# Performance work log

Hardware: AMD Instinct MI355X
Metric: run time of the kernel (lower is better)

## Reference

```python
import jax, jax.numpy as jnp
import numpy as np

EPS = 1e-5
G, N, H, P, K = 8, 128, 64, 64, 4  # n_groups, d_state, n_heads, head_dim, conv kernel
R = H // G  # heads per group


def _rmsnorm(x, w, eps=EPS):
    return x * jax.lax.rsqrt(jnp.mean(x * x, axis=-1, keepdims=True) + eps) * w


def setup_inputs() -> dict:
    key = jax.random.key(0)
    ks = jax.random.split(key, 8)
    B, L, Dm = 2, 1024, 2048
    d_inner = 2 * Dm                      # 4096
    conv_dim = d_inner + 2 * G * N        # 6144
    proj_dim = 2 * d_inner + 2 * G * N + H  # 10304
    return {
        "hidden_states": jax.random.normal(ks[0], (B, L, Dm), jnp.float32),
        "residual": jax.random.normal(ks[1], (B, L, Dm), jnp.float32),
        "norm_w": jnp.ones((Dm,), jnp.float32),
        "in_proj_w": jax.random.normal(ks[2], (proj_dim, Dm), jnp.float32) * 0.02,
        "conv_w": jax.random.normal(ks[3], (conv_dim, K), jnp.float32) * 0.1,
        "conv_b": jnp.zeros((conv_dim,), jnp.float32),
        "A_log": jnp.log(jnp.arange(1, H + 1, dtype=jnp.float32)),
        "D_param": jnp.ones((H,), jnp.float32),
        "dt_bias": jax.random.uniform(ks[4], (H,), jnp.float32, -4.0, -1.0),
        "gate_norm_w": jnp.ones((d_inner,), jnp.float32),
        "out_proj_w": jax.random.normal(ks[5], (Dm, d_inner), jnp.float32) * 0.02,
    }


def reference(hidden_states, residual, norm_w, in_proj_w, conv_w, conv_b,
              A_log, D_param, dt_bias, gate_norm_w, out_proj_w):
    B, L, Dm = hidden_states.shape
    d_inner = 2 * Dm
    conv_dim = d_inner + 2 * G * N

    # fused residual-add RMSNorm (residual is not None branch)
    h = hidden_states + residual
    new_residual = h
    x = _rmsnorm(h, norm_w)

    # in_proj -> [z | xBC | dt]
    proj = jnp.einsum('bld,ed->ble', x, in_proj_w)
    z = proj[..., :d_inner]
    xBC = proj[..., d_inner:d_inner + conv_dim]
    dt = proj[..., d_inner + conv_dim:]            # [B, L, H]

    # causal depthwise conv1d over xBC, then SiLU
    lhs = jnp.transpose(xBC, (0, 2, 1))            # [B, C, L]
    rhs = conv_w[:, None, :]                       # [C, 1, K]
    conv = jax.lax.conv_general_dilated(
        lhs, rhs, window_strides=(1,), padding=[(K - 1, 0)],
        feature_group_count=conv_dim)
    xBC = jax.nn.silu(jnp.transpose(conv, (0, 2, 1)) + conv_b)

    xs = xBC[..., :d_inner].reshape(B, L, G, R, P)   # per-head inputs
    Bm = xBC[..., d_inner:d_inner + G * N].reshape(B, L, G, N)
    Cm = xBC[..., d_inner + G * N:].reshape(B, L, G, N)

    dt = jax.nn.softplus(dt + dt_bias)               # [B, L, H]
    A = -jnp.exp(A_log)                              # [H]
    dA = jnp.exp(dt * A).reshape(B, L, G, R)
    dtg = dt.reshape(B, L, G, R)

    # time-major for scan
    def step(hst, inp):
        dA_t, dt_t, x_t, B_t, C_t = inp            # [B,G,R], [B,G,R], [B,G,R,P], [B,G,N], [B,G,N]
        dBx = jnp.einsum('bgr,bgn,bgrp->bgrpn', dt_t, B_t, x_t)
        hst = hst * dA_t[..., None, None] + dBx    # [B,G,R,P,N]
        y_t = jnp.einsum('bgrpn,bgn->bgrp', hst, C_t)
        return hst, y_t

    tm = lambda a: jnp.moveaxis(a, 1, 0)
    h0 = jnp.zeros((B, G, R, P, N), hidden_states.dtype)
    _, ys = jax.lax.scan(step, h0, (tm(dA), tm(dtg), tm(xs), tm(Bm), tm(Cm)))
    y = jnp.moveaxis(ys, 0, 1)                     # [B, L, G, R, P]
    y = y + D_param.reshape(G, R)[None, None, :, :, None] * xs
    y = y.reshape(B, L, d_inner)

    # gated RMSNorm then out_proj
    y = _rmsnorm(y * jax.nn.silu(z), gate_norm_w)
    out = jnp.einsum('ble,de->bld', y, out_proj_w)
    return out, new_residual
```

## Files before the change

kernel.cpp:

```cpp
#include <hip/hip_runtime.h>

#define TOK 2048
#define DM 2048
#define DI 4096
#define NG 8
#define NN 128
#define PROJ_D 10304
#define PROJ_P 10496
#define CONV_D 6144
#define LSEQ 1024
#define CHUNK 64
#define NCHUNK 16

typedef unsigned short u16;
typedef __attribute__((ext_vector_type(4))) float f32x4;
typedef __attribute__((ext_vector_type(8))) short s16x8;
typedef __attribute__((ext_vector_type(4))) unsigned short u16x4;

__device__ __forceinline__ u16 f2bf(float f) {
  union { float f; unsigned u; } x; x.f = f;
  unsigned r = (x.u + 0x7FFFu + ((x.u >> 16) & 1u)) >> 16;
  return (u16)r;
}
__device__ __forceinline__ float bf2f(u16 u) {
  union { unsigned u; float f; } x; x.u = ((unsigned)u) << 16; return x.f;
}

__device__ __forceinline__ float blockReduceSum256(float s) {
  __shared__ float red[4];
  #pragma unroll
  for (int o = 32; o > 0; o >>= 1) s += __shfl_down(s, o, 64);
  int lane = threadIdx.x & 63, wid = threadIdx.x >> 6;
  if (lane == 0) red[wid] = s;
  __syncthreads();
  return red[0] + red[1] + red[2] + red[3];
}

__global__ __launch_bounds__(256) void cvt_bf16_pad(const float* __restrict__ src, u16* __restrict__ dst,
                                                    long n_src, long n_dst) {
  long i = ((long)blockIdx.x * 256 + threadIdx.x) * 4;
  if (i >= n_dst) return;
  u16x4 o;
  if (i < n_src) {
    f32x4 v = *(const f32x4*)&src[i];
    o.x = f2bf(v.x); o.y = f2bf(v.y); o.z = f2bf(v.z); o.w = f2bf(v.w);
  } else {
    o.x = 0; o.y = 0; o.z = 0; o.w = 0;
  }
  *(u16x4*)&dst[i] = o;
}

__global__ __launch_bounds__(256) void addnorm_kernel(const float* __restrict__ hs, const float* __restrict__ res,
        const float* __restrict__ w, float* __restrict__ nres, u16* __restrict__ xbf) {
  int row = blockIdx.x;
  size_t base = (size_t)row * DM;
  int tid = threadIdx.x;
  f32x4 h[2];
  float s = 0.f;
  #pragma unroll
  for (int i = 0; i < 2; i++) {
    int off = i * 1024 + tid * 4;
    f32x4 a = *(const f32x4*)&hs[base + off];
    f32x4 b = *(const f32x4*)&res[base + off];
    f32x4 v = a + b;
    h[i] = v;
    *(f32x4*)&nres[base + off] = v;
    s += v.x * v.x + v.y * v.y + v.z * v.z + v.w * v.w;
  }
  s = blockReduceSum256(s);
  float rs = rsqrtf(s * (1.f / DM) + 1e-5f);
  #pragma unroll
  for (int i = 0; i < 2; i++) {
    int off = i * 1024 + tid * 4;
    f32x4 wv = *(const f32x4*)&w[off];
    f32x4 v = h[i];
    u16x4 o;
    o.x = f2bf(v.x * rs * wv.x);
    o.y = f2bf(v.y * rs * wv.y);
    o.z = f2bf(v.z * rs * wv.z);
    o.w = f2bf(v.w * rs * wv.w);
    *(u16x4*)&xbf[base + off] = o;
  }
}

__device__ __forceinline__ void gld_lds16(const void* g, void* l) {
  __builtin_amdgcn_global_load_lds((const __attribute__((address_space(1))) void*)g,
                                   (__attribute__((address_space(3))) void*)l, 16, 0, 0);
}

template <bool BF16OUT>
__global__ __launch_bounds__(512, 4) void gemm32(const u16* __restrict__ A, const u16* __restrict__ Bw,
                                                 void* __restrict__ Cv, int K, int Cstride, int nbx) {
  __shared__ u16 As[3][128][32];
  __shared__ u16 Bs[3][256][32];
  int tid = threadIdx.x;
  int lane = tid & 63, w = tid >> 6;
  int wr = w >> 2, wc = w & 3;
  int cpx = gridDim.x >> 3;
  int bid = blockIdx.x;
  int lb = (bid & 7) * cpx + (bid >> 3);
  int by = lb / nbx, bx = lb - by * nbx;
  size_t m0 = (size_t)by * 128, n0 = (size_t)bx * 256;
  const u16* Ab = A + m0 * K;
  const u16* Bb = Bw + n0 * K;

  f32x4 acc[4][4];
  #pragma unroll
  for (int i = 0; i < 4; ++i)
    #pragma unroll
    for (int j = 0; j < 4; ++j) acc[i][j] = (f32x4){0.f, 0.f, 0.f, 0.f};

  int fr = lane & 15, fq = lane >> 4;
  int lrow = lane >> 2, lg = lane & 3;

  auto S = [&](int kt) {
    int bu = kt % 3;
    {
      int row = w * 16 + lrow;
      int cs = (lg ^ ((row >> 1) & 3)) * 8;
      gld_lds16(Ab + (size_t)row * K + kt * 32 + cs, &As[bu][w * 16][0]);
    }
    #pragma unroll
    for (int j = 0; j < 2; ++j) {
      int row = j * 128 + w * 16 + lrow;
      int cs = (lg ^ ((row >> 1) & 3)) * 8;
      gld_lds16(Bb + (size_t)row * K + kt * 32 + cs, &Bs[bu][j * 128 + w * 16][0]);
    }
  };

  int nkt = K >> 5;
  S(0); S(1);
  asm volatile("s_waitcnt vmcnt(3)" ::: "memory");
  __builtin_amdgcn_s_barrier();

  for (int kt = 0; kt < nkt; ++kt) {
    int bu = kt % 3;
    s16x8 a[4], b[4];
    #pragma unroll
    for (int mi = 0; mi < 4; ++mi) {
      int row = wr * 64 + mi * 16 + fr;
      a[mi] = *(const s16x8*)&As[bu][row][(fq ^ ((row >> 1) & 3)) * 8];
    }
    #pragma unroll
    for (int ni = 0; ni < 4; ++ni) {
      int row = wc * 64 + ni * 16 + fr;
      b[ni] = *(const s16x8*)&Bs[bu][row][(fq ^ ((row >> 1) & 3)) * 8];
    }
    if (kt + 2 < nkt) {
      S(kt + 2);
      asm volatile("s_waitcnt vmcnt(3)" ::: "memory");
    } else {
      asm volatile("s_waitcnt vmcnt(0)" ::: "memory");
    }
    __builtin_amdgcn_s_barrier();
    __builtin_amdgcn_s_setprio(1);
    #pragma unroll
    for (int mi = 0; mi < 4; ++mi)
      #pragma unroll
      for (int ni = 0; ni < 4; ++ni)
        acc[mi][ni] = __builtin_amdgcn_mfma_f32_16x16x32_bf16(a[mi], b[ni], acc[mi][ni], 0, 0, 0);
    __builtin_amdgcn_s_setprio(0);
    __builtin_amdgcn_s_barrier();
  }
  size_t crow0 = m0 + wr * 64 + fq * 4;
  size_t ccol0 = n0 + wc * 64 + fr;
  if constexpr (BF16OUT) {
    u16* C = (u16*)Cv;
    #pragma unroll
    for (int mi = 0; mi < 4; ++mi)
      #pragma unroll
      for (int ni = 0; ni < 4; ++ni)
        #pragma unroll
        for (int j = 0; j < 4; ++j)
          C[(crow0 + mi * 16 + j) * Cstride + ccol0 + ni * 16] = f2bf(acc[mi][ni][j]);
  } else {
    float* C = (float*)Cv;
    #pragma unroll
    for (int mi = 0; mi < 4; ++mi)
      #pragma unroll
      for (int ni = 0; ni < 4; ++ni)
        #pragma unroll
        for (int j = 0; j < 4; ++j)
          C[(crow0 + mi * 16 + j) * Cstride + ccol0 + ni * 16] = acc[mi][ni][j];
  }
}

template <bool BF16OUT>
__global__ __launch_bounds__(512, 2) void gemm8p(const u16* __restrict__ A, const u16* __restrict__ Bw,
                                                 void* __restrict__ Cv, int K, int Cstride, int nbx,
                                                 int nks, size_t part_stride) {
  __shared__ u16 As[2][256][64];
  __shared__ u16 Bs[2][256][64];
  int tid = threadIdx.x;
  int lane = tid & 63, w = tid >> 6;
  int wr = w >> 2, wc = w & 3;
  int cpx = gridDim.x >> 3;
  int bid = blockIdx.x;
  int lb = (bid & 7) * cpx + (bid >> 3);
  int ks = lb % nks;
  int tile = lb / nks;
  int by = tile / nbx, bx = tile - by * nbx;
  int Ks = K / nks;
  int k0 = ks * Ks;
  size_t m0 = (size_t)by * 256, n0 = (size_t)bx * 256;
  const u16* Ab = A + m0 * K;
  const u16* Bb = Bw + n0 * K;

  f32x4 acc[8][4];
  #pragma unroll
  for (int i = 0; i < 8; ++i)
    #pragma unroll
    for (int j = 0; j < 4; ++j) acc[i][j] = (f32x4){0.f, 0.f, 0.f, 0.f};

  int l3 = lane >> 3;
  int colsw = ((lane & 7) ^ l3) << 3;
  int fr = lane & 15, fq = lane >> 4;
  int pc0 = (fq * 8) ^ ((fr & 7) << 3);
  int pc1 = pc0 ^ 32;

  auto S = [&](int kt, int mat, int half) {
    int d = kt & 1;
    const u16* src = mat ? Bb : Ab;
    u16* dstbase = mat ? &Bs[d][0][0] : &As[d][0][0];
    #pragma unroll
    for (int j = 0; j < 2; ++j) {
      int rb = half * 128 + (w * 2 + j) * 8;
      gld_lds16(src + (size_t)(rb + l3) * K + k0 + kt * 64 + colsw, dstbase + rb * 64);
    }
  };

  int nkt = Ks >> 6;
  S(0, 1, 0); S(0, 1, 1); S(0, 0, 0); S(0, 0, 1);
  S(1, 1, 0); S(1, 1, 1);
  asm volatile("s_waitcnt vmcnt(4)" ::: "memory");
  __builtin_amdgcn_s_barrier();

  for (int kt = 0; kt < nkt; ++kt) {
    int d = kt & 1;
    s16x8 b[4][2];
    #pragma unroll
    for (int q = 0; q < 4; ++q) {
      if (q == 0) {
        #pragma unroll
        for (int ni = 0; ni < 4; ++ni) {
          b[ni][0] = *(const s16x8*)&Bs[d][wc * 64 + ni * 16 + fr][pc0];
          b[ni][1] = *(const s16x8*)&Bs[d][wc * 64 + ni * 16 + fr][pc1];
        }
      }
      s16x8 a[2][2];
      #pragma unroll
      for (int mi = 0; mi < 2; ++mi) {
        a[mi][0] = *(const s16x8*)&As[d][wr * 128 + q * 32 + mi * 16 + fr][pc0];
        a[mi][1] = *(const s16x8*)&As[d][wr * 128 + q * 32 + mi * 16 + fr][pc1];
      }
      if (q == 0)      { if (kt + 1 < nkt) S(kt + 1, 0, 0); }
      else if (q == 1) { if (kt + 1 < nkt) S(kt + 1, 0, 1); }
      else if (q == 2) { if (kt + 2 < nkt) S(kt + 2, 1, 0); }
      else {
        if (kt + 2 < nkt) { S(kt + 2, 1, 1); asm volatile("s_waitcnt vmcnt(4)" ::: "memory"); }
        else              { asm volatile("s_waitcnt vmcnt(0)" ::: "memory"); }
      }
      __builtin_amdgcn_s_barrier();
      __builtin_amdgcn_s_setprio(1);
      #pragma unroll
      for (int mi = 0; mi < 2; ++mi)
        #pragma unroll
        for (int ni = 0; ni < 4; ++ni) {
          acc[q * 2 + mi][ni] = __builtin_amdgcn_mfma_f32_16x16x32_bf16(a[mi][0], b[ni][0], acc[q * 2 + mi][ni], 0, 0, 0);
          acc[q * 2 + mi][ni] = __builtin_amdgcn_mfma_f32_16x16x32_bf16(a[mi][1], b[ni][1], acc[q * 2 + mi][ni], 0, 0, 0);
        }
      __builtin_amdgcn_s_setprio(0);
      __builtin_amdgcn_s_barrier();
    }
  }
  size_t crow0 = m0 + wr * 128 + fq * 4;
  size_t ccol0 = n0 + wc * 64 + fr;
  if constexpr (BF16OUT) {
    u16* C = (u16*)Cv;
    #pragma unroll
    for (int mf = 0; mf < 8; ++mf)
      #pragma unroll
      for (int ni = 0; ni < 4; ++ni)
        #pragma unroll
        for (int j = 0; j < 4; ++j)
          C[(crow0 + mf * 16 + j) * Cstride + ccol0 + ni * 16] = f2bf(acc[mf][ni][j]);
  } else {
    float* C = (float*)Cv + (size_t)ks * part_stride;
    #pragma unroll
    for (int mf = 0; mf < 8; ++mf)
      #pragma unroll
      for (int ni = 0; ni < 4; ++ni)
        #pragma unroll
        for (int j = 0; j < 4; ++j)
          C[(crow0 + mf * 16 + j) * Cstride + ccol0 + ni * 16] = acc[mf][ni][j];
  }
}

__global__ __launch_bounds__(256) void reduce4_kernel(const float* __restrict__ part, float* __restrict__ out) {
  size_t i = ((size_t)blockIdx.x * 256 + threadIdx.x) * 4;
  const size_t st = (size_t)TOK * DM;
  f32x4 s = *(const f32x4*)&part[i];
  s += *(const f32x4*)&part[i + st];
  s += *(const f32x4*)&part[i + 2 * st];
  s += *(const f32x4*)&part[i + 3 * st];
  *(f32x4*)&out[i] = s;
}

__global__ __launch_bounds__(256) void conv_silu_kernel(const u16* __restrict__ proj,
        const float* __restrict__ cw, const float* __restrict__ cb, u16* __restrict__ xbc) {
  long gid = (long)blockIdx.x * 256 + threadIdx.x;
  int c4 = (int)(gid % 1536);
  long t = gid / 1536;
  int l = (int)(t & 1023);
  int c = c4 * 4;
  const u16* base = proj + (size_t)t * PROJ_P + DI + c;
  f32x4 acc = *(const f32x4*)&cb[c];
  f32x4 w0 = *(const f32x4*)&cw[(c + 0) * 4];
  f32x4 w1 = *(const f32x4*)&cw[(c + 1) * 4];
  f32x4 w2 = *(const f32x4*)&cw[(c + 2) * 4];
  f32x4 w3 = *(const f32x4*)&cw[(c + 3) * 4];
  #pragma unroll
  for (int k = 0; k < 4; k++) {
    int ls = l - 3 + k;
    if (ls >= 0) {
      u16x4 v = *(const u16x4*)(base + ((long)(k - 3)) * PROJ_P);
      acc.x = fmaf(bf2f(v.x), w0[k], acc.x);
      acc.y = fmaf(bf2f(v.y), w1[k], acc.y);
      acc.z = fmaf(bf2f(v.z), w2[k], acc.z);
      acc.w = fmaf(bf2f(v.w), w3[k], acc.w);
    }
  }
  u16x4 o;
  o.x = f2bf(acc.x / (1.f + expf(-acc.x)));
  o.y = f2bf(acc.y / (1.f + expf(-acc.y)));
  o.z = f2bf(acc.z / (1.f + expf(-acc.z)));
  o.w = f2bf(acc.w / (1.f + expf(-acc.w)));
  *(u16x4*)&xbc[(size_t)t * CONV_D + c] = o;
}

__global__ __launch_bounds__(256) void dt_kernel(const u16* __restrict__ proj, const float* __restrict__ dt_bias,
        const float* __restrict__ A_log, float* __restrict__ dtspT, float* __restrict__ dtaT) {
  int idx = blockIdx.x * 256 + threadIdx.x;
  int t = idx >> 6, hh = idx & 63;
  int b = t >> 10, l = t & 1023;
  float dtv = bf2f(proj[(size_t)t * PROJ_P + (DI + CONV_D) + hh]) + dt_bias[hh];
  float sp = (dtv > 15.f) ? dtv : log1pf(expf(dtv));
  float Ah = -expf(A_log[hh]);
  size_t o = (size_t)(b * 64 + hh) * LSEQ + l;
  dtspT[o] = sp;
  dtaT[o] = sp * Ah;
}

__global__ __launch_bounds__(512) void ssd_kernel(const u16* __restrict__ xbc, const float* __restrict__ dtsp,
        const float* __restrict__ dta, const float* __restrict__ Dp, u16* __restrict__ y) {
  int bid = blockIdx.x;
  int g = bid & 7, b = (bid >> 3) & 1, r = (bid >> 4) & 7, ph = bid >> 7;
  int h = g * 8 + r;
  int p0 = ph * 32;
  int tid = threadIdx.x;
  int w = tid >> 6, lane = tid & 63;

  __shared__ u16 Bsh[2][64][128];
  __shared__ u16 Csh[2][64][128];
  __shared__ u16 Xt[2][32][64];
  __shared__ u16 Btw[2][128][64];
  __shared__ u16 GWsh[64][64];
  __shared__ u16 Hbf[32][128];
  __shared__ float dtsh[LSEQ];
  __shared__ float Lsh[LSEQ];

  const float* dtrow = dtsp + (size_t)(b * 64 + h) * LSEQ;
  const float* dtarow = dta + (size_t)(b * 64 + h) * LSEQ;
  if (tid < 256) { f32x4 v = *(const f32x4*)&dtrow[tid * 4]; *(f32x4*)&dtsh[tid * 4] = v; }
  for (int cc = w; cc < NCHUNK; cc += 8) {
    float a = dtarow[cc * 64 + lane];
    #pragma unroll
    for (int o = 1; o < 64; o <<= 1) { float t2 = __shfl_up(a, o, 64); if (lane >= o) a += t2; }
    Lsh[cc * 64 + lane] = a;
  }
  {
    u16* hp = &Hbf[0][0];
    for (int i = tid; i < 1024; i += 512) *(u16x4*)&hp[i * 4] = (u16x4){0, 0, 0, 0};
  }
  float Dv = Dp[h];
  const u16* xb = xbc + (size_t)b * LSEQ * CONV_D;
  int swz = (lane & 7) << 3;
  __syncthreads();

  auto stage = [&](int cc, int d) {
    int t0c = cc * 64;
    int pw = w - 4, ptid = tid - 256;
    #pragma unroll
    for (int q = 0; q < 4; ++q) {
      int rowb = pw * 16 + q * 4;
      int row = rowb + (lane >> 4);
      int colb = ((lane & 15) * 8) ^ ((row & 7) << 3);
      gld_lds16(xb + (size_t)(t0c + row) * CONV_D + DI + g * 128 + colb, &Bsh[d][rowb][0]);
      gld_lds16(xb + (size_t)(t0c + row) * CONV_D + DI + NG * NN + g * 128 + colb, &Csh[d][rowb][0]);
    }
    {
      int s = ptid & 63, pq = ptid >> 6;
      const u16* xr = xb + (size_t)(t0c + s) * CONV_D + g * 512 + r * 64 + p0;
      #pragma unroll
      for (int pb = 0; pb < 2; ++pb) {
        int pl0 = pb * 16 + pq * 4;
        u16x4 v = *(const u16x4*)&xr[pl0];
        #pragma unroll
        for (int j = 0; j < 4; ++j) {
          int p = pl0 + j;
          Xt[d][p][s ^ ((p & 7) << 3)] = v[j];
        }
      }
    }
    {
      int s = ptid & 63, nq = ptid >> 6;
      float wend = __expf(Lsh[t0c + 63] - Lsh[t0c + s]) * dtsh[t0c + s];
      const u16* br = xb + (size_t)(t0c + s) * CONV_D + DI + g * 128;
      #pragma unroll
      for (int nb = 0; nb < 8; ++nb) {
        int n0 = nb * 16 + nq * 4;
        u16x4 v = *(const u16x4*)&br[n0];
        #pragma unroll
        for (int j = 0; j < 4; ++j) {
          int n = n0 + j;
          Btw[d][n][s ^ ((n & 7) << 3)] = f2bf(bf2f(v[j]) * wend);
        }
      }
    }
  };

  if (w >= 4) stage(0, 0);
  __syncthreads();

  f32x4 hst[2][2];
  #pragma unroll
  for (int i = 0; i < 2; ++i)
    #pragma unroll
    for (int j = 0; j < 2; ++j) hst[i][j] = (f32x4){0.f, 0.f, 0.f, 0.f};

  for (int c = 0; c < NCHUNK; ++c) {
    int d = c & 1;
    int t0c = c * 64;
    if (w >= 4) {
      if (c + 1 < NCHUNK) stage(c + 1, d ^ 1);
    } else {
      s16x8 aC[4];
      #pragma unroll
      for (int k = 0; k < 4; ++k)
        aC[k] = *(const s16x8*)&Csh[d][w * 16 + (lane & 15)][(k * 32 + (lane >> 4) * 8) ^ swz];
      f32x4 Gacc[4];
      #pragma unroll
      for (int st = 0; st < 4; ++st) Gacc[st] = (f32x4){0.f, 0.f, 0.f, 0.f};
      #pragma unroll
      for (int st = 0; st < 4; ++st)
        #pragma unroll
        for (int k = 0; k < 4; ++k) {
          s16x8 bB = *(const s16x8*)&Bsh[d][st * 16 + (lane & 15)][(k * 32 + (lane >> 4) * 8) ^ swz];
          Gacc[st] = __builtin_amdgcn_mfma_f32_16x16x32_bf16(aC[k], bB, Gacc[st], 0, 0, 0);
        }
      #pragma unroll
      for (int st = 0; st < 4; ++st) {
        int s = st * 16 + (lane & 15);
        float Ls = Lsh[t0c + s], dts = dtsh[t0c + s];
        #pragma unroll
        for (int j = 0; j < 4; ++j) {
          int t = w * 16 + (lane >> 4) * 4 + j;
          float wgt = (s <= t) ? __expf(Lsh[t0c + t] - Ls) * dts : 0.f;
          GWsh[t][s ^ ((t & 7) << 3)] = f2bf(Gacc[st][j] * wgt);
        }
      }
      f32x4 Yacc[2], Y2acc[2];
      #pragma unroll
      for (int pt = 0; pt < 2; ++pt) { Yacc[pt] = (f32x4){0.f,0.f,0.f,0.f}; Y2acc[pt] = (f32x4){0.f,0.f,0.f,0.f}; }
      s16x8 aGW[2];
      #pragma unroll
      for (int k = 0; k < 2; ++k)
        aGW[k] = *(const s16x8*)&GWsh[w * 16 + (lane & 15)][(k * 32 + (lane >> 4) * 8) ^ swz];
      #pragma unroll
      for (int pt = 0; pt < 2; ++pt) {
        #pragma unroll
        for (int k = 0; k < 2; ++k) {
          s16x8 bX = *(const s16x8*)&Xt[d][pt * 16 + (lane & 15)][(k * 32 + (lane >> 4) * 8) ^ swz];
          Yacc[pt] = __builtin_amdgcn_mfma_f32_16x16x32_bf16(aGW[k], bX, Yacc[pt], 0, 0, 0);
        }
        #pragma unroll
        for (int k = 0; k < 4; ++k) {
          s16x8 bH = *(const s16x8*)&Hbf[pt * 16 + (lane & 15)][(k * 32 + (lane >> 4) * 8) ^ swz];
          Y2acc[pt] = __builtin_amdgcn_mfma_f32_16x16x32_bf16(aC[k], bH, Y2acc[pt], 0, 0, 0);
        }
      }
      float el[4];
      #pragma unroll
      for (int j = 0; j < 4; ++j) el[j] = __expf(Lsh[t0c + w * 16 + (lane >> 4) * 4 + j]);
      #pragma unroll
      for (int pt = 0; pt < 2; ++pt) {
        int p = pt * 16 + (lane & 15);
        #pragma unroll
        for (int j = 0; j < 4; ++j) {
          int t = w * 16 + (lane >> 4) * 4 + j;
          float xv = bf2f(Xt[d][p][t ^ ((p & 7) << 3)]);
          float yv = Yacc[pt][j] + el[j] * Y2acc[pt][j] + Dv * xv;
          y[((size_t)b * LSEQ + t0c + t) * DI + g * 512 + r * 64 + p0 + p] = f2bf(yv);
        }
      }
      float e63 = __expf(Lsh[t0c + 63]);
      s16x8 aX[2][2];
      #pragma unroll
      for (int mp = 0; mp < 2; ++mp)
        #pragma unroll
        for (int k = 0; k < 2; ++k)
          aX[mp][k] = *(const s16x8*)&Xt[d][mp * 16 + (lane & 15)][(k * 32 + (lane >> 4) * 8) ^ swz];
      #pragma unroll
      for (int mp = 0; mp < 2; ++mp)
        #pragma unroll
        for (int nn = 0; nn < 2; ++nn) {
          #pragma unroll
          for (int j = 0; j < 4; ++j) hst[mp][nn][j] *= e63;
          #pragma unroll
          for (int k = 0; k < 2; ++k) {
            s16x8 bW = *(const s16x8*)&Btw[d][w * 32 + nn * 16 + (lane & 15)][(k * 32 + (lane >> 4) * 8) ^ swz];
            hst[mp][nn] = __builtin_amdgcn_mfma_f32_16x16x32_bf16(aX[mp][k], bW, hst[mp][nn], 0, 0, 0);
          }
        }
    }
    __syncthreads();
    if (w < 4) {
      #pragma unroll
      for (int mp = 0; mp < 2; ++mp)
        #pragma unroll
        for (int nn = 0; nn < 2; ++nn) {
          int n = w * 32 + nn * 16 + (lane & 15);
          #pragma unroll
          for (int j = 0; j < 4; ++j) {
            int p = mp * 16 + (lane >> 4) * 4 + j;
            Hbf[p][n ^ ((p & 7) << 3)] = f2bf(hst[mp][nn][j]);
          }
        }
    }
    __syncthreads();
  }
}

__global__ __launch_bounds__(256) void gate_kernel(const u16* __restrict__ y, const u16* __restrict__ proj,
        const float* __restrict__ gw, u16* __restrict__ y2) {
  int row = blockIdx.x;
  const u16* yr = y + (size_t)row * DI;
  const u16* zr = proj + (size_t)row * PROJ_P;
  int tid = threadIdx.x;
  f32x4 v[4];
  float s = 0.f;
  #pragma unroll
  for (int i = 0; i < 4; i++) {
    int off = i * 1024 + tid * 4;
    u16x4 av = *(const u16x4*)&yr[off];
    u16x4 zv = *(const u16x4*)&zr[off];
    f32x4 t;
    float z0 = bf2f(zv.x), z1 = bf2f(zv.y), z2 = bf2f(zv.z), z3 = bf2f(zv.w);
    t.x = bf2f(av.x) * (z0 / (1.f + expf(-z0)));
    t.y = bf2f(av.y) * (z1 / (1.f + expf(-z1)));
    t.z = bf2f(av.z) * (z2 / (1.f + expf(-z2)));
    t.w = bf2f(av.w) * (z3 / (1.f + expf(-z3)));
    v[i] = t;
    s += t.x * t.x + t.y * t.y + t.z * t.z + t.w * t.w;
  }
  s = blockReduceSum256(s);
  float rs = rsqrtf(s * (1.f / DI) + 1e-5f);
  #pragma unroll
  for (int i = 0; i < 4; i++) {
    int off = i * 1024 + tid * 4;
    f32x4 wv = *(const f32x4*)&gw[off];
    u16x4 o;
    o.x = f2bf(v[i].x * rs * wv.x);
    o.y = f2bf(v[i].y * rs * wv.y);
    o.z = f2bf(v[i].z * rs * wv.z);
    o.w = f2bf(v[i].w * rs * wv.w);
    *(u16x4*)&y2[(size_t)row * DI + off] = o;
  }
}

extern "C" void kernel_launch(void* const* d_in, const int* in_sizes, int n_in,
                              void* d_out, int out_size, void* d_ws, size_t ws_size,
                              hipStream_t stream) {
  (void)in_sizes; (void)n_in; (void)out_size; (void)ws_size;
  const float* hs      = (const float*)d_in[0];
  const float* res     = (const float*)d_in[1];
  const float* norm_w  = (const float*)d_in[2];
  const float* w_in    = (const float*)d_in[3];
  const float* conv_w  = (const float*)d_in[4];
  const float* conv_b  = (const float*)d_in[5];
  const float* A_log   = (const float*)d_in[6];
  const float* D_param = (const float*)d_in[7];
  const float* dt_bias = (const float*)d_in[8];
  const float* gate_w  = (const float*)d_in[9];
  const float* w_out   = (const float*)d_in[10];

  float* out  = (float*)d_out;
  float* nres = out + (size_t)TOK * DM;

  char* ws = (char*)d_ws;
  size_t off = 0;
  u16*   WB1  = (u16*)(ws + off);   off += (size_t)PROJ_P * DM * 2;
  u16*   WB2  = (u16*)(ws + off);   off += (size_t)DM * DI * 2;
  u16*   XBF  = (u16*)(ws + off);   off += (size_t)TOK * DM * 2;
  u16*   PROJ = (u16*)(ws + off);   off += (size_t)TOK * PROJ_P * 2;
  u16*   XBC  = (u16*)(ws + off);   off += (size_t)TOK * CONV_D * 2;
  float* DTSP = (float*)(ws + off); off += (size_t)TOK * 64 * 4;
  float* DTA  = (float*)(ws + off); off += (size_t)TOK * 64 * 4;
  u16*   Y    = (u16*)(ws + off);   off += (size_t)TOK * DI * 2;
  u16*   Y2   = (u16*)(ws + off);   off += (size_t)TOK * DI * 2;
  float* PART = (float*)(ws + off); off += (size_t)4 * TOK * DM * 4;

  cvt_bf16_pad<<<20992, 256, 0, stream>>>(w_in, WB1, (long)PROJ_D * DM, (long)PROJ_P * DM);
  cvt_bf16_pad<<<8192, 256, 0, stream>>>(w_out, WB2, (long)DM * DI, (long)DM * DI);
  addnorm_kernel<<<TOK, 256, 0, stream>>>(hs, res, norm_w, nres, XBF);
  gemm32<true><<<(TOK / 128) * (PROJ_P / 256), 512, 0, stream>>>(XBF, WB1, PROJ, DM, PROJ_P, PROJ_P / 256);
  conv_silu_kernel<<<(TOK * (CONV_D / 4)) / 256, 256, 0, stream>>>(PROJ, conv_w, conv_b, XBC);
  dt_kernel<<<(TOK * 64) / 256, 256, 0, stream>>>(PROJ, dt_bias, A_log, DTSP, DTA);
  ssd_kernel<<<256, 512, 0, stream>>>(XBC, DTSP, DTA, D_param, Y);
  gate_kernel<<<TOK, 256, 0, stream>>>(Y, PROJ, gate_w, Y2);
  gemm8p<false><<<(TOK / 256) * (DM / 256) * 4, 512, 0, stream>>>(Y2, WB2, PART, DI, DM, DM / 256, 4, (size_t)TOK * DM);
  reduce4_kernel<<<(TOK * DM) / 1024, 256, 0, stream>>>(PART, out);
}
```

Before: 308.0 us.

## Store split-K partials in bf16, reorder GEMM tile raster, double-buffer SSD state

The out_proj split-K GEMM now writes its partial sums as bf16 rather than fp32, which halves the partial-buffer writes and the reads in the reduce kernel. The cost is rounding each partial to bf16 before the sum. The in_proj GEMM rasterisation changes so consecutive blocks walk down M for a fixed N tile, aiming for better weight-tile reuse in cache. In the SSD kernel the inter-chunk state buffer is double-buffered, which removes one __syncthreads per chunk.

```diff
diff --git a/kernel.cpp b/kernel.cpp
--- a/kernel.cpp
+++ b/kernel.cpp
@@ -88,9 +88,8 @@
                                    (__attribute__((address_space(3))) void*)l, 16, 0, 0);
 }
 
-template <bool BF16OUT>
 __global__ __launch_bounds__(512, 4) void gemm32(const u16* __restrict__ A, const u16* __restrict__ Bw,
-                                                 void* __restrict__ Cv, int K, int Cstride, int nbx) {
+                                                 u16* __restrict__ C, int K, int Cstride, int nby) {
   __shared__ u16 As[3][128][32];
   __shared__ u16 Bs[3][256][32];
   int tid = threadIdx.x;
@@ -99,7 +98,7 @@
   int cpx = gridDim.x >> 3;
   int bid = blockIdx.x;
   int lb = (bid & 7) * cpx + (bid >> 3);
-  int by = lb / nbx, bx = lb - by * nbx;
+  int by = lb % nby, bx = lb / nby;
   size_t m0 = (size_t)by * 128, n0 = (size_t)bx * 256;
   const u16* Ab = A + m0 * K;
   const u16* Bb = Bw + n0 * K;
@@ -164,30 +163,18 @@
   }
   size_t crow0 = m0 + wr * 64 + fq * 4;
   size_t ccol0 = n0 + wc * 64 + fr;
-  if constexpr (BF16OUT) {
-    u16* C = (u16*)Cv;
-    #pragma unroll
-    for (int mi = 0; mi < 4; ++mi)
-      #pragma unroll
-      for (int ni = 0; ni < 4; ++ni)
-        #pragma unroll
-        for (int j = 0; j < 4; ++j)
-          C[(crow0 + mi * 16 + j) * Cstride + ccol0 + ni * 16] = f2bf(acc[mi][ni][j]);
-  } else {
-    float* C = (float*)Cv;
-    #pragma unroll
-    for (int mi = 0; mi < 4; ++mi)
-      #pragma unroll
-      for (int ni = 0; ni < 4; ++ni)
-        #pragma unroll
-        for (int j = 0; j < 4; ++j)
-          C[(crow0 + mi * 16 + j) * Cstride + ccol0 + ni * 16] = acc[mi][ni][j];
-  }
-}
-
-template <bool BF16OUT>
+  #pragma unroll
+  for (int mi = 0; mi < 4; ++mi)
+    #pragma unroll
+    for (int ni = 0; ni < 4; ++ni)
+      #pragma unroll
+      for (int j = 0; j < 4; ++j)
+        C[(crow0 + mi * 16 + j) * Cstride + ccol0 + ni * 16] = f2bf(acc[mi][ni][j]);
+}
+
+template <bool KSPLIT>
 __global__ __launch_bounds__(512, 2) void gemm8p(const u16* __restrict__ A, const u16* __restrict__ Bw,
-                                                 void* __restrict__ Cv, int K, int Cstride, int nbx,
+                                                 u16* __restrict__ C, int K, int Cstride, int nby,
                                                  int nks, size_t part_stride) {
   __shared__ u16 As[2][256][64];
   __shared__ u16 Bs[2][256][64];
@@ -197,10 +184,16 @@
   int cpx = gridDim.x >> 3;
   int bid = blockIdx.x;
   int lb = (bid & 7) * cpx + (bid >> 3);
-  int ks = lb % nks;
-  int tile = lb / nks;
-  int by = tile / nbx, bx = tile - by * nbx;
-  int Ks = K / nks;
+  int ks, by, bx;
+  if constexpr (KSPLIT) {
+    ks = lb % nks;
+    int tile = lb / nks;
+    by = tile / nby; bx = tile - by * nby;
+  } else {
+    ks = 0;
+    by = lb % nby; bx = lb / nby;
+  }
+  int Ks = KSPLIT ? (K / nks) : K;
   int k0 = ks * Ks;
   size_t m0 = (size_t)by * 256, n0 = (size_t)bx * 256;
   const u16* Ab = A + m0 * K;
@@ -275,34 +268,28 @@
   }
   size_t crow0 = m0 + wr * 128 + fq * 4;
   size_t ccol0 = n0 + wc * 64 + fr;
-  if constexpr (BF16OUT) {
-    u16* C = (u16*)Cv;
-    #pragma unroll
-    for (int mf = 0; mf < 8; ++mf)
-      #pragma unroll
-      for (int ni = 0; ni < 4; ++ni)
-        #pragma unroll
-        for (int j = 0; j < 4; ++j)
-          C[(crow0 + mf * 16 + j) * Cstride + ccol0 + ni * 16] = f2bf(acc[mf][ni][j]);
-  } else {
-    float* C = (float*)Cv + (size_t)ks * part_stride;
-    #pragma unroll
-    for (int mf = 0; mf < 8; ++mf)
-      #pragma unroll
-      for (int ni = 0; ni < 4; ++ni)
-        #pragma unroll
-        for (int j = 0; j < 4; ++j)
-          C[(crow0 + mf * 16 + j) * Cstride + ccol0 + ni * 16] = acc[mf][ni][j];
-  }
-}
-
-__global__ __launch_bounds__(256) void reduce4_kernel(const float* __restrict__ part, float* __restrict__ out) {
+  u16* Co = KSPLIT ? (C + (size_t)ks * part_stride) : C;
+  #pragma unroll
+  for (int mf = 0; mf < 8; ++mf)
+    #pragma unroll
+    for (int ni = 0; ni < 4; ++ni)
+      #pragma unroll
+      for (int j = 0; j < 4; ++j)
+        Co[(crow0 + mf * 16 + j) * Cstride + ccol0 + ni * 16] = f2bf(acc[mf][ni][j]);
+}
+
+__global__ __launch_bounds__(256) void reduce4_kernel(const u16* __restrict__ part, float* __restrict__ out) {
   size_t i = ((size_t)blockIdx.x * 256 + threadIdx.x) * 4;
   const size_t st = (size_t)TOK * DM;
-  f32x4 s = *(const f32x4*)&part[i];
-  s += *(const f32x4*)&part[i + st];
-  s += *(const f32x4*)&part[i + 2 * st];
-  s += *(const f32x4*)&part[i + 3 * st];
+  u16x4 p0 = *(const u16x4*)&part[i];
+  u16x4 p1 = *(const u16x4*)&part[i + st];
+  u16x4 p2 = *(const u16x4*)&part[i + 2 * st];
+  u16x4 p3 = *(const u16x4*)&part[i + 3 * st];
+  f32x4 s;
+  s.x = bf2f(p0.x) + bf2f(p1.x) + bf2f(p2.x) + bf2f(p3.x);
+  s.y = bf2f(p0.y) + bf2f(p1.y) + bf2f(p2.y) + bf2f(p3.y);
+  s.z = bf2f(p0.z) + bf2f(p1.z) + bf2f(p2.z) + bf2f(p3.z);
+  s.w = bf2f(p0.w) + bf2f(p1.w) + bf2f(p2.w) + bf2f(p3.w);
   *(f32x4*)&out[i] = s;
 }
 
@@ -365,7 +352,7 @@
   __shared__ u16 Xt[2][32][64];
   __shared__ u16 Btw[2][128][64];
   __shared__ u16 GWsh[64][64];
-  __shared__ u16 Hbf[32][128];
+  __shared__ u16 Hbf[2][32][128];
   __shared__ float dtsh[LSEQ];
   __shared__ float Lsh[LSEQ];
 
@@ -379,7 +366,7 @@
     Lsh[cc * 64 + lane] = a;
   }
   {
-    u16* hp = &Hbf[0][0];
+    u16* hp = &Hbf[0][0][0];
     for (int i = tid; i < 1024; i += 512) *(u16x4*)&hp[i * 4] = (u16x4){0, 0, 0, 0};
   }
   float Dv = Dp[h];
@@ -440,6 +427,7 @@
 
   for (int c = 0; c < NCHUNK; ++c) {
     int d = c & 1;
+    int ch = c & 1;
     int t0c = c * 64;
     if (w >= 4) {
       if (c + 1 < NCHUNK) stage(c + 1, d ^ 1);
@@ -485,7 +473,7 @@
         }
         #pragma unroll
         for (int k = 0; k < 4; ++k) {
-          s16x8 bH = *(const s16x8*)&Hbf[pt * 16 + (lane & 15)][(k * 32 + (lane >> 4) * 8) ^ swz];
+          s16x8 bH = *(const s16x8*)&Hbf[ch][pt * 16 + (lane & 15)][(k * 32 + (lane >> 4) * 8) ^ swz];
           Y2acc[pt] = __builtin_amdgcn_mfma_f32_16x16x32_bf16(aC[k], bH, Y2acc[pt], 0, 0, 0);
         }
       }
@@ -522,9 +510,6 @@
             hst[mp][nn] = __builtin_amdgcn_mfma_f32_16x16x32_bf16(aX[mp][k], bW, hst[mp][nn], 0, 0, 0);
           }
         }
-    }
-    __syncthreads();
-    if (w < 4) {
       #pragma unroll
       for (int mp = 0; mp < 2; ++mp)
         #pragma unroll
@@ -533,7 +518,7 @@
           #pragma unroll
           for (int j = 0; j < 4; ++j) {
             int p = mp * 16 + (lane >> 4) * 4 + j;
-            Hbf[p][n ^ ((p & 7) << 3)] = f2bf(hst[mp][nn][j]);
+            Hbf[ch ^ 1][p][n ^ ((p & 7) << 3)] = f2bf(hst[mp][nn][j]);
           }
         }
     }
@@ -608,16 +593,16 @@
   float* DTA  = (float*)(ws + off); off += (size_t)TOK * 64 * 4;
   u16*   Y    = (u16*)(ws + off);   off += (size_t)TOK * DI * 2;
   u16*   Y2   = (u16*)(ws + off);   off += (size_t)TOK * DI * 2;
-  float* PART = (float*)(ws + off); off += (size_t)4 * TOK * DM * 4;
+  u16*   PART = (u16*)(ws + off);   off += (size_t)4 * TOK * DM * 2;
 
   cvt_bf16_pad<<<20992, 256, 0, stream>>>(w_in, WB1, (long)PROJ_D * DM, (long)PROJ_P * DM);
   cvt_bf16_pad<<<8192, 256, 0, stream>>>(w_out, WB2, (long)DM * DI, (long)DM * DI);
   addnorm_kernel<<<TOK, 256, 0, stream>>>(hs, res, norm_w, nres, XBF);
-  gemm32<true><<<(TOK / 128) * (PROJ_P / 256), 512, 0, stream>>>(XBF, WB1, PROJ, DM, PROJ_P, PROJ_P / 256);
+  gemm32<<<(TOK / 128) * (PROJ_P / 256), 512, 0, stream>>>(XBF, WB1, PROJ, DM, PROJ_P, TOK / 128);
   conv_silu_kernel<<<(TOK * (CONV_D / 4)) / 256, 256, 0, stream>>>(PROJ, conv_w, conv_b, XBC);
   dt_kernel<<<(TOK * 64) / 256, 256, 0, stream>>>(PROJ, dt_bias, A_log, DTSP, DTA);
   ssd_kernel<<<256, 512, 0, stream>>>(XBC, DTSP, DTA, D_param, Y);
   gate_kernel<<<TOK, 256, 0, stream>>>(Y, PROJ, gate_w, Y2);
-  gemm8p<false><<<(TOK / 256) * (DM / 256) * 4, 512, 0, stream>>>(Y2, WB2, PART, DI, DM, DM / 256, 4, (size_t)TOK * DM);
+  gemm8p<true><<<(TOK / 256) * (DM / 256) * 4, 512, 0, stream>>>(Y2, WB2, PART, DI, DM, DM / 256, 4, (size_t)TOK * DM);
   reduce4_kernel<<<(TOK * DM) / 1024, 256, 0, stream>>>(PART, out);
 }
```

Result: faster. 281.9 us, median of 2 (-8.4%).
